# Optimization experiments

Hardware: AMD Instinct MI355X
Metric: run time of the kernel (lower is better)

The kernel has to match this reference:

```python
import jax, jax.numpy as jnp
import numpy as np

N_EMBED = 1024
HEAD_SIZE = 64


def setup_inputs() -> dict:
    key = jax.random.key(0)
    kx, kk, kq, kv = jax.random.split(key, 4)
    B, T = 8, 2048
    x = jax.random.normal(kx, (B, T, N_EMBED), dtype=jnp.float32)
    # nn.Linear weights, stored as (in, out) so projection is x @ W
    s = 1.0 / np.sqrt(N_EMBED)
    Wk = jax.random.uniform(kk, (N_EMBED, HEAD_SIZE), jnp.float32, -s, s)
    Wq = jax.random.uniform(kq, (N_EMBED, HEAD_SIZE), jnp.float32, -s, s)
    Wv = jax.random.uniform(kv, (N_EMBED, HEAD_SIZE), jnp.float32, -s, s)
    return {"x": x, "Wk": Wk, "Wq": Wq, "Wv": Wv}


def reference(x, Wk, Wq, Wv):
    # x: [B, T, C] with C = n_embed
    C = x.shape[-1]
    k = x @ Wk  # [B, T, H]
    q = x @ Wq  # [B, T, H]
    v = x @ Wv  # [B, T, H]
    # NOTE: original scales by n_embed**-0.5, not head_size**-0.5
    wei = jnp.einsum("bth,bsh->bts", q, k) * (C ** -0.5)  # [B, T, T]
    wei = jax.nn.softmax(wei, axis=-1)
    # dropout = 0.0 (eval mode) -> identity
    out = jnp.einsum("bts,bsh->bth", wei, v)  # [B, T, H]
    return out
```

## Files before the change

### kernel.cpp

```cpp
#include <hip/hip_runtime.h>
#include <stdint.h>


#define B_ 8
#define T_ 2048
#define C_ 1024
#define H_ 64

typedef float f32x4 __attribute__((ext_vector_type(4)));
typedef short s16x8 __attribute__((ext_vector_type(8)));

__device__ __forceinline__ unsigned int rhu16(float f) {
    return (__float_as_uint(f) + 0x8000u) >> 16;
}
__device__ __forceinline__ unsigned int pkbf(float lo, float hi) {
    unsigned int a = __float_as_uint(lo) + 0x8000u;
    unsigned int b = __float_as_uint(hi) + 0x8000u;
    return __builtin_amdgcn_perm(b, a, 0x07060302u);
}
__device__ __forceinline__ void ld_lds16(const void* g, void* l) {
    __builtin_amdgcn_global_load_lds(
        (const __attribute__((address_space(1))) unsigned int*)g,
        (__attribute__((address_space(3))) unsigned int*)l, 16, 0, 0);
}

__global__ __launch_bounds__(256) void wconv(const float* __restrict__ Wk,
        const float* __restrict__ Wq, const float* __restrict__ Wv,
        unsigned short* __restrict__ Wt) {
    __shared__ float ls[64 * 65];
    const int bx = blockIdx.x, t = threadIdx.x;
    const int mat = bx >> 4, c0 = (bx & 15) << 6;
    const float* W = (mat == 0) ? Wk : ((mat == 1) ? Wq : Wv);
    const float sc = (mat == 1) ? 0.03125f : 1.0f;
    #pragma unroll
    for (int k = 0; k < 4; k++) {
        int i = t + (k << 8);
        int cr = i >> 4, hq = (i & 15) << 2;
        float4 v = *reinterpret_cast<const float4*>(&W[(size_t)(c0 + cr) * H_ + hq]);
        ls[cr * 65 + hq + 0] = v.x; ls[cr * 65 + hq + 1] = v.y;
        ls[cr * 65 + hq + 2] = v.z; ls[cr * 65 + hq + 3] = v.w;
    }
    __syncthreads();
    #pragma unroll
    for (int k = 0; k < 4; k++) {
        int i = t + (k << 8);
        int h = i >> 4, cq = (i & 15) << 2;
        float a = ls[(cq + 0) * 65 + h] * sc, b = ls[(cq + 1) * 65 + h] * sc;
        float c = ls[(cq + 2) * 65 + h] * sc, d = ls[(cq + 3) * 65 + h] * sc;
        uint2 o; o.x = pkbf(a, b); o.y = pkbf(c, d);
        *reinterpret_cast<uint2*>(&Wt[(size_t)(mat * 64 + h) * C_ + c0 + cq]) = o;
    }
}

__global__ __launch_bounds__(128, 2) void qkv(const float* __restrict__ x,
        const unsigned short* __restrict__ Wt,
        unsigned short* __restrict__ kb, unsigned short* __restrict__ qb,
        unsigned short* __restrict__ vtb) {
    const int t = threadIdx.x, lane = t & 63, w = t >> 6;
    const int l15 = lane & 15, quad = lane >> 4;
    const int m0 = blockIdx.x * 32;
    const int bb = m0 >> 11;
    const int colw = w * 96;

    const char* xq0 = (const char*)(x + (size_t)(m0 + l15) * C_ + quad * 8);
    const char* xq1 = xq0 + (size_t)16 * C_ * 4;
    const char* wq[6];
    #pragma unroll
    for (int ct = 0; ct < 6; ct++)
        wq[ct] = (const char*)(Wt + (size_t)(colw + ct * 16 + l15) * C_ + quad * 8);

    f32x4 acc[2][6];
    #pragma unroll
    for (int rt = 0; rt < 2; rt++)
        #pragma unroll
        for (int ct = 0; ct < 6; ct++)
            #pragma unroll
            for (int j = 0; j < 4; j++) acc[rt][ct][j] = 0.0f;

    float4 xr[3][2][2][2];
    #pragma unroll
    for (int cc = 0; cc < 2; cc++) {
        #pragma unroll
        for (int ks = 0; ks < 2; ks++)
            #pragma unroll
            for (int h = 0; h < 2; h++) {
                xr[cc][0][ks][h] = *reinterpret_cast<const float4*>(
                    xq0 + cc * 256 + ks * 128 + h * 16);
                xr[cc][1][ks][h] = *reinterpret_cast<const float4*>(
                    xq1 + cc * 256 + ks * 128 + h * 16);
            }
    }

    #pragma unroll
    for (int c = 0; c < 16; c++) {
        __builtin_amdgcn_sched_barrier(0);
        if (c < 14) {
            const int sl = (c + 2) % 3, off = (c + 2) * 256;
            #pragma unroll
            for (int ks = 0; ks < 2; ks++)
                #pragma unroll
                for (int h = 0; h < 2; h++) {
                    xr[sl][0][ks][h] = *reinterpret_cast<const float4*>(
                        xq0 + off + ks * 128 + h * 16);
                    xr[sl][1][ks][h] = *reinterpret_cast<const float4*>(
                        xq1 + off + ks * 128 + h * 16);
                }
        }
        uint4 wr[6][2];
        #pragma unroll
        for (int ct = 0; ct < 6; ct++)
            #pragma unroll
            for (int ks = 0; ks < 2; ks++)
                wr[ct][ks] = *reinterpret_cast<const uint4*>(
                    wq[ct] + c * 128 + ks * 64);
        __builtin_amdgcn_sched_barrier(0);

        const int cs = c % 3;
        s16x8 af[2][2];
        #pragma unroll
        for (int rt = 0; rt < 2; rt++)
            #pragma unroll
            for (int ks = 0; ks < 2; ks++) {
                const float4 a = xr[cs][rt][ks][0], b = xr[cs][rt][ks][1];
                uint4 pk;
                pk.x = pkbf(a.x, a.y); pk.y = pkbf(a.z, a.w);
                pk.z = pkbf(b.x, b.y); pk.w = pkbf(b.z, b.w);
                af[rt][ks] = *reinterpret_cast<s16x8*>(&pk);
            }
        #pragma unroll
        for (int ks = 0; ks < 2; ks++)
            #pragma unroll
            for (int rt = 0; rt < 2; rt++)
                #pragma unroll
                for (int ct = 0; ct < 6; ct++)
                    acc[rt][ct] = __builtin_amdgcn_mfma_f32_16x16x32_bf16(
                        af[rt][ks],
                        *reinterpret_cast<s16x8*>(&wr[ct][ks]),
                        acc[rt][ct], 0, 0, 0);
    }

    #pragma unroll
    for (int ct = 0; ct < 6; ct++) {
        int cb = colw + ct * 16;
        int sel = cb >> 6;
        int h = (cb & 63) + l15;
        #pragma unroll
        for (int rt = 0; rt < 2; rt++) {
            int row0 = m0 + rt * 16 + quad * 4;
            if (sel < 2) {
                unsigned short* dst = sel ? qb : kb;
                #pragma unroll
                for (int r = 0; r < 4; r++)
                    dst[(size_t)(row0 + r) * H_ + h] = (unsigned short)rhu16(acc[rt][ct][r]);
            } else {
                int tt = row0 - bb * T_;
                uint2 pk;
                pk.x = pkbf(acc[rt][ct][0], acc[rt][ct][1]);
                pk.y = pkbf(acc[rt][ct][2], acc[rt][ct][3]);
                *reinterpret_cast<uint2*>(&vtb[((size_t)bb * H_ + h) * T_ + tt]) = pk;
            }
        }
    }
}

__global__ __launch_bounds__(256, 2) void attn(
        const unsigned short* __restrict__ qb,
        const unsigned short* __restrict__ kb,
        const unsigned short* __restrict__ vtb,
        float* __restrict__ out) {
    __shared__ __align__(16) char smem[75776];

    const int t = threadIdx.x, lane = t & 63, w = t >> 6;
    const int l15 = lane & 15, quad = lane >> 4;
    const int bb = blockIdx.x & 7;
    const int q0 = (blockIdx.x >> 3) << 5;
    const size_t kbase = (size_t)bb * T_ * H_;
    char* Kb = smem + w * 16384;
    char* Vb = Kb + 8192;
    unsigned short* Pw = (unsigned short*)(smem + 65536 + w * 2560);

    s16x8 qf[2][2];
    #pragma unroll
    for (int rt = 0; rt < 2; rt++)
        #pragma unroll
        for (int ks = 0; ks < 2; ks++)
            qf[rt][ks] = *reinterpret_cast<const s16x8*>(
                &qb[kbase + (size_t)(q0 + rt * 16 + l15) * H_ + ks * 32 + quad * 8]);

    const unsigned short* kp = kb + kbase;
    const unsigned short* vp = vtb + (size_t)bb * H_ * T_;
    size_t kg[4], vg[4]; int kl[4], vl[4];
    #pragma unroll
    for (int g = 0; g < 4; g++) {
        kg[g] = (size_t)(g * 8 + (lane & 7)) * H_ + (lane >> 3) * 8;
        kl[g] = g * 1024 + lane * 16;
        vg[g] = (size_t)(g * 16 + l15) * T_ + quad * 8;
        vl[g] = g * 1024 + lane * 16;
    }

    const int sw = w << 9;
    #pragma unroll
    for (int g = 0; g < 4; g++) ld_lds16(kp + (size_t)sw * H_ + kg[g], Kb + kl[g]);
    #pragma unroll
    for (int g = 0; g < 4; g++) ld_lds16(vp + sw + vg[g], Vb + vl[g]);

    f32x4 oacc[2][4];
    #pragma unroll
    for (int rt = 0; rt < 2; rt++)
        #pragma unroll
        for (int ht = 0; ht < 4; ht++)
            #pragma unroll
            for (int j = 0; j < 4; j++) oacc[rt][ht][j] = 0.0f;
    float l_run[2] = {0.0f, 0.0f};
    const f32x4 z4 = {0.0f, 0.0f, 0.0f, 0.0f};

    for (int it = 0; it < 16; it++) {
        const int cb = it & 1;
        if (it < 15) {
            const int sn = sw + (it + 1) * 32;
            char* Kn = Kb + (cb ^ 1) * 4096;
            char* Vn = Vb + (cb ^ 1) * 4096;
            #pragma unroll
            for (int g = 0; g < 4; g++) ld_lds16(kp + (size_t)sn * H_ + kg[g], Kn + kl[g]);
            #pragma unroll
            for (int g = 0; g < 4; g++) ld_lds16(vp + sn + vg[g], Vn + vl[g]);
            __builtin_amdgcn_sched_barrier(0);
            __builtin_amdgcn_s_waitcnt(0x0f78);
        } else {
            __builtin_amdgcn_s_waitcnt(0x0f70);
        }
        __builtin_amdgcn_sched_barrier(0);

        const unsigned short* Kc = (const unsigned short*)(Kb + cb * 4096);
        const unsigned short* Vc = (const unsigned short*)(Vb + cb * 4096);

        s16x8 kf[2][2], vf[4];
        #pragma unroll
        for (int st = 0; st < 2; st++)
            #pragma unroll
            for (int ks = 0; ks < 2; ks++) {
                int s = st * 16 + l15;
                kf[st][ks] = *reinterpret_cast<const s16x8*>(
                    Kc + (s >> 3) * 512 + ((4 * ks + quad) * 8 + (s & 7)) * 8);
            }
        #pragma unroll
        for (int ht = 0; ht < 4; ht++)
            vf[ht] = *reinterpret_cast<const s16x8*>(
                Vc + ht * 512 + (quad * 16 + l15) * 8);

        f32x4 sacc[2][2];
        #pragma unroll
        for (int rt = 0; rt < 2; rt++)
            #pragma unroll
            for (int st = 0; st < 2; st++) {
                f32x4 s0v = __builtin_amdgcn_mfma_f32_16x16x32_bf16(kf[st][0], qf[rt][0], z4, 0, 0, 0);
                sacc[rt][st] = __builtin_amdgcn_mfma_f32_16x16x32_bf16(kf[st][1], qf[rt][1], s0v, 0, 0, 0);
            }

        #pragma unroll
        for (int rt = 0; rt < 2; rt++) {
            float ls = 0.0f;
            #pragma unroll
            for (int st = 0; st < 2; st++) {
                float p0 = __expf(sacc[rt][st][0]);
                float p1 = __expf(sacc[rt][st][1]);
                float p2 = __expf(sacc[rt][st][2]);
                float p3 = __expf(sacc[rt][st][3]);
                ls += (p0 + p1) + (p2 + p3);
                uint2 pk; pk.x = pkbf(p0, p1); pk.y = pkbf(p2, p3);
                *reinterpret_cast<uint2*>(
                    &Pw[(rt * 16 + l15) * 40 + st * 16 + quad * 4]) = pk;
            }
            l_run[rt] += ls;
        }

        #pragma unroll
        for (int rt = 0; rt < 2; rt++) {
            s16x8 pf = *reinterpret_cast<const s16x8*>(&Pw[(rt * 16 + l15) * 40 + quad * 8]);
            #pragma unroll
            for (int ht = 0; ht < 4; ht++)
                oacc[rt][ht] = __builtin_amdgcn_mfma_f32_16x16x32_bf16(
                    pf, vf[ht], oacc[rt][ht], 0, 0, 0);
        }
    }

    #pragma unroll
    for (int rt = 0; rt < 2; rt++) {
        l_run[rt] += __shfl_xor(l_run[rt], 16);
        l_run[rt] += __shfl_xor(l_run[rt], 32);
    }

    __syncthreads();
    float* Osf = (float*)smem;
    float* Ls  = (float*)smem + 3 * 32 * 66;
    if (w > 0) {
        int wi = w - 1;
        #pragma unroll
        for (int rt = 0; rt < 2; rt++) {
            if (quad == 0) Ls[wi * 32 + rt * 16 + l15] = l_run[rt];
            #pragma unroll
            for (int ht = 0; ht < 4; ht++)
                #pragma unroll
                for (int r = 0; r < 4; r++)
                    Osf[wi * 2112 + (rt * 16 + quad * 4 + r) * 66 + ht * 16 + l15] = oacc[rt][ht][r];
        }
    }
    __syncthreads();
    if (w == 0) {
        #pragma unroll
        for (int rt = 0; rt < 2; rt++)
            #pragma unroll
            for (int r = 0; r < 4; r++) {
                int row = rt * 16 + quad * 4 + r;
                float lt = __shfl(l_run[rt], quad * 4 + r)
                         + Ls[0 * 32 + row] + Ls[1 * 32 + row] + Ls[2 * 32 + row];
                float inv = 1.0f / lt;
                #pragma unroll
                for (int ht = 0; ht < 4; ht++) {
                    float o = oacc[rt][ht][r]
                            + Osf[0 * 2112 + row * 66 + ht * 16 + l15]
                            + Osf[1 * 2112 + row * 66 + ht * 16 + l15]
                            + Osf[2 * 2112 + row * 66 + ht * 16 + l15];
                    out[kbase + (size_t)(q0 + row) * H_ + ht * 16 + l15] = o * inv;
                }
            }
    }
}

extern "C" void kernel_launch(void* const* d_in, const int* in_sizes, int n_in,
                              void* d_out, int out_size, void* d_ws, size_t ws_size,
                              hipStream_t stream) {
    const float* x  = (const float*)d_in[0];
    const float* Wk = (const float*)d_in[1];
    const float* Wq = (const float*)d_in[2];
    const float* Wv = (const float*)d_in[3];

    unsigned short* kb  = (unsigned short*)d_ws;
    unsigned short* qbf = kb  + (size_t)B_ * T_ * H_;
    unsigned short* vtb = qbf + (size_t)B_ * T_ * H_;
    unsigned short* Wt  = (unsigned short*)d_out;

    wconv<<<48,  256, 0, stream>>>(Wk, Wq, Wv, Wt);
    qkv  <<<512, 128, 0, stream>>>(x, Wt, kb, qbf, vtb);
    attn <<<512, 256, 0, stream>>>(qbf, kb, vtb, (float*)d_out);
}
```

Baseline: 160.5 us.

## Load attention K/V fragments directly into registers and split qkv across four waves

The attention kernel drops the async global-to-LDS staging of K and V tiles and instead loads MFMA fragments straight from global memory into a double-buffered register set, prefetching two iterations ahead. This shrinks shared memory use, which may allow more blocks per CU. The qkv projection kernel moves to 256 threads with each wave owning a 16-row by 96-column tile, and it double-buffers both x and weight fragments in registers. The cost is more register pressure and less coalesced global loads, which now depend on cache hits instead of shared staging.

```diff
diff --git a/kernel.cpp b/kernel.cpp
--- a/kernel.cpp
+++ b/kernel.cpp
@@ -17,11 +17,6 @@
     unsigned int a = __float_as_uint(lo) + 0x8000u;
     unsigned int b = __float_as_uint(hi) + 0x8000u;
     return __builtin_amdgcn_perm(b, a, 0x07060302u);
-}
-__device__ __forceinline__ void ld_lds16(const void* g, void* l) {
-    __builtin_amdgcn_global_load_lds(
-        (const __attribute__((address_space(1))) unsigned int*)g,
-        (__attribute__((address_space(3))) unsigned int*)l, 16, 0, 0);
 }
 
 __global__ __launch_bounds__(256) void wconv(const float* __restrict__ Wk,
@@ -52,91 +47,80 @@
     }
 }
 
-__global__ __launch_bounds__(128, 2) void qkv(const float* __restrict__ x,
+__global__ __launch_bounds__(256, 2) void qkv(const float* __restrict__ x,
         const unsigned short* __restrict__ Wt,
         unsigned short* __restrict__ kb, unsigned short* __restrict__ qb,
         unsigned short* __restrict__ vtb) {
     const int t = threadIdx.x, lane = t & 63, w = t >> 6;
+    const int rw = w >> 1, cw = w & 1;
     const int l15 = lane & 15, quad = lane >> 4;
     const int m0 = blockIdx.x * 32;
     const int bb = m0 >> 11;
-    const int colw = w * 96;
-
-    const char* xq0 = (const char*)(x + (size_t)(m0 + l15) * C_ + quad * 8);
-    const char* xq1 = xq0 + (size_t)16 * C_ * 4;
-    const char* wq[6];
+    const int colw = cw * 96;
+
+    const char* xp = (const char*)(x + (size_t)(m0 + rw * 16 + l15) * C_ + quad * 8);
+    const char* wp[6];
     #pragma unroll
     for (int ct = 0; ct < 6; ct++)
-        wq[ct] = (const char*)(Wt + (size_t)(colw + ct * 16 + l15) * C_ + quad * 8);
-
-    f32x4 acc[2][6];
-    #pragma unroll
-    for (int rt = 0; rt < 2; rt++)
+        wp[ct] = (const char*)(Wt + (size_t)(colw + ct * 16 + l15) * C_ + quad * 8);
+
+    f32x4 acc[6];
+    #pragma unroll
+    for (int ct = 0; ct < 6; ct++)
+        #pragma unroll
+        for (int j = 0; j < 4; j++) acc[ct][j] = 0.0f;
+
+    float4 xr[2][4];
+    uint4  wr[2][6][2];
+
+    #pragma unroll
+    for (int p = 0; p < 2; p++) {
+        xr[p][0] = *reinterpret_cast<const float4*>(xp + p * 256 + 0);
+        xr[p][1] = *reinterpret_cast<const float4*>(xp + p * 256 + 16);
+        xr[p][2] = *reinterpret_cast<const float4*>(xp + p * 256 + 128);
+        xr[p][3] = *reinterpret_cast<const float4*>(xp + p * 256 + 144);
         #pragma unroll
         for (int ct = 0; ct < 6; ct++)
             #pragma unroll
-            for (int j = 0; j < 4; j++) acc[rt][ct][j] = 0.0f;
-
-    float4 xr[3][2][2][2];
-    #pragma unroll
-    for (int cc = 0; cc < 2; cc++) {
+            for (int ks = 0; ks < 2; ks++)
+                wr[p][ct][ks] = *reinterpret_cast<const uint4*>(
+                    wp[ct] + p * 128 + ks * 64);
+    }
+
+    #pragma unroll
+    for (int c = 0; c < 16; c++) {
+        const int cb = c & 1;
+        s16x8 af[2];
+        #pragma unroll
+        for (int ks = 0; ks < 2; ks++) {
+            const float4 a = xr[cb][ks * 2 + 0], b = xr[cb][ks * 2 + 1];
+            uint4 pk;
+            pk.x = pkbf(a.x, a.y); pk.y = pkbf(a.z, a.w);
+            pk.z = pkbf(b.x, b.y); pk.w = pkbf(b.z, b.w);
+            af[ks] = *reinterpret_cast<s16x8*>(&pk);
+        }
         #pragma unroll
         for (int ks = 0; ks < 2; ks++)
             #pragma unroll
-            for (int h = 0; h < 2; h++) {
-                xr[cc][0][ks][h] = *reinterpret_cast<const float4*>(
-                    xq0 + cc * 256 + ks * 128 + h * 16);
-                xr[cc][1][ks][h] = *reinterpret_cast<const float4*>(
-                    xq1 + cc * 256 + ks * 128 + h * 16);
-            }
-    }
-
-    #pragma unroll
-    for (int c = 0; c < 16; c++) {
+            for (int ct = 0; ct < 6; ct++)
+                acc[ct] = __builtin_amdgcn_mfma_f32_16x16x32_bf16(
+                    af[ks], *reinterpret_cast<s16x8*>(&wr[cb][ct][ks]),
+                    acc[ct], 0, 0, 0);
         __builtin_amdgcn_sched_barrier(0);
         if (c < 14) {
-            const int sl = (c + 2) % 3, off = (c + 2) * 256;
-            #pragma unroll
-            for (int ks = 0; ks < 2; ks++)
+            const int o = (c + 2) * 256, ow = (c + 2) * 128;
+            xr[cb][0] = *reinterpret_cast<const float4*>(xp + o + 0);
+            xr[cb][1] = *reinterpret_cast<const float4*>(xp + o + 16);
+            xr[cb][2] = *reinterpret_cast<const float4*>(xp + o + 128);
+            xr[cb][3] = *reinterpret_cast<const float4*>(xp + o + 144);
+            #pragma unroll
+            for (int ct = 0; ct < 6; ct++)
                 #pragma unroll
-                for (int h = 0; h < 2; h++) {
-                    xr[sl][0][ks][h] = *reinterpret_cast<const float4*>(
-                        xq0 + off + ks * 128 + h * 16);
-                    xr[sl][1][ks][h] = *reinterpret_cast<const float4*>(
-                        xq1 + off + ks * 128 + h * 16);
-                }
-        }
-        uint4 wr[6][2];
-        #pragma unroll
-        for (int ct = 0; ct < 6; ct++)
-            #pragma unroll
-            for (int ks = 0; ks < 2; ks++)
-                wr[ct][ks] = *reinterpret_cast<const uint4*>(
-                    wq[ct] + c * 128 + ks * 64);
+                for (int ks = 0; ks < 2; ks++)
+                    wr[cb][ct][ks] = *reinterpret_cast<const uint4*>(
+                        wp[ct] + ow + ks * 64);
+        }
         __builtin_amdgcn_sched_barrier(0);
-
-        const int cs = c % 3;
-        s16x8 af[2][2];
-        #pragma unroll
-        for (int rt = 0; rt < 2; rt++)
-            #pragma unroll
-            for (int ks = 0; ks < 2; ks++) {
-                const float4 a = xr[cs][rt][ks][0], b = xr[cs][rt][ks][1];
-                uint4 pk;
-                pk.x = pkbf(a.x, a.y); pk.y = pkbf(a.z, a.w);
-                pk.z = pkbf(b.x, b.y); pk.w = pkbf(b.z, b.w);
-                af[rt][ks] = *reinterpret_cast<s16x8*>(&pk);
-            }
-        #pragma unroll
-        for (int ks = 0; ks < 2; ks++)
-            #pragma unroll
-            for (int rt = 0; rt < 2; rt++)
-                #pragma unroll
-                for (int ct = 0; ct < 6; ct++)
-                    acc[rt][ct] = __builtin_amdgcn_mfma_f32_16x16x32_bf16(
-                        af[rt][ks],
-                        *reinterpret_cast<s16x8*>(&wr[ct][ks]),
-                        acc[rt][ct], 0, 0, 0);
     }
 
     #pragma unroll
@@ -144,21 +128,18 @@
         int cb = colw + ct * 16;
         int sel = cb >> 6;
         int h = (cb & 63) + l15;
-        #pragma unroll
-        for (int rt = 0; rt < 2; rt++) {
-            int row0 = m0 + rt * 16 + quad * 4;
-            if (sel < 2) {
-                unsigned short* dst = sel ? qb : kb;
-                #pragma unroll
-                for (int r = 0; r < 4; r++)
-                    dst[(size_t)(row0 + r) * H_ + h] = (unsigned short)rhu16(acc[rt][ct][r]);
-            } else {
-                int tt = row0 - bb * T_;
-                uint2 pk;
-                pk.x = pkbf(acc[rt][ct][0], acc[rt][ct][1]);
-                pk.y = pkbf(acc[rt][ct][2], acc[rt][ct][3]);
-                *reinterpret_cast<uint2*>(&vtb[((size_t)bb * H_ + h) * T_ + tt]) = pk;
-            }
+        int row0 = m0 + rw * 16 + quad * 4;
+        if (sel < 2) {
+            unsigned short* dst = sel ? qb : kb;
+            #pragma unroll
+            for (int r = 0; r < 4; r++)
+                dst[(size_t)(row0 + r) * H_ + h] = (unsigned short)rhu16(acc[ct][r]);
+        } else {
+            int tt = row0 - bb * T_;
+            uint2 pk;
+            pk.x = pkbf(acc[ct][0], acc[ct][1]);
+            pk.y = pkbf(acc[ct][2], acc[ct][3]);
+            *reinterpret_cast<uint2*>(&vtb[((size_t)bb * H_ + h) * T_ + tt]) = pk;
         }
     }
 }
@@ -168,16 +149,14 @@
         const unsigned short* __restrict__ kb,
         const unsigned short* __restrict__ vtb,
         float* __restrict__ out) {
-    __shared__ __align__(16) char smem[75776];
+    __shared__ __align__(16) char smem[25728];
 
     const int t = threadIdx.x, lane = t & 63, w = t >> 6;
     const int l15 = lane & 15, quad = lane >> 4;
     const int bb = blockIdx.x & 7;
     const int q0 = (blockIdx.x >> 3) << 5;
     const size_t kbase = (size_t)bb * T_ * H_;
-    char* Kb = smem + w * 16384;
-    char* Vb = Kb + 8192;
-    unsigned short* Pw = (unsigned short*)(smem + 65536 + w * 2560);
+    unsigned short* Pw = (unsigned short*)(smem + w * 2560);
 
     s16x8 qf[2][2];
     #pragma unroll
@@ -187,22 +166,27 @@
             qf[rt][ks] = *reinterpret_cast<const s16x8*>(
                 &qb[kbase + (size_t)(q0 + rt * 16 + l15) * H_ + ks * 32 + quad * 8]);
 
-    const unsigned short* kp = kb + kbase;
-    const unsigned short* vp = vtb + (size_t)bb * H_ * T_;
-    size_t kg[4], vg[4]; int kl[4], vl[4];
-    #pragma unroll
-    for (int g = 0; g < 4; g++) {
-        kg[g] = (size_t)(g * 8 + (lane & 7)) * H_ + (lane >> 3) * 8;
-        kl[g] = g * 1024 + lane * 16;
-        vg[g] = (size_t)(g * 16 + l15) * T_ + quad * 8;
-        vl[g] = g * 1024 + lane * 16;
-    }
-
     const int sw = w << 9;
-    #pragma unroll
-    for (int g = 0; g < 4; g++) ld_lds16(kp + (size_t)sw * H_ + kg[g], Kb + kl[g]);
-    #pragma unroll
-    for (int g = 0; g < 4; g++) ld_lds16(vp + sw + vg[g], Vb + vl[g]);
+    const unsigned short* kq = kb + kbase + (size_t)(sw + l15) * H_ + quad * 8;
+    const unsigned short* vq[4];
+    #pragma unroll
+    for (int ht = 0; ht < 4; ht++)
+        vq[ht] = vtb + ((size_t)bb * H_ + ht * 16 + l15) * T_ + sw + quad * 8;
+
+    s16x8 kfb[2][2][2], vfb[2][4];
+    #pragma unroll
+    for (int p = 0; p < 2; p++) {
+        const unsigned short* kc = kq + (size_t)p * 2048;
+        #pragma unroll
+        for (int st = 0; st < 2; st++)
+            #pragma unroll
+            for (int ks = 0; ks < 2; ks++)
+                kfb[p][st][ks] = *reinterpret_cast<const s16x8*>(
+                    kc + st * 1024 + ks * 32);
+        #pragma unroll
+        for (int ht = 0; ht < 4; ht++)
+            vfb[p][ht] = *reinterpret_cast<const s16x8*>(vq[ht] + p * 32);
+    }
 
     f32x4 oacc[2][4];
     #pragma unroll
@@ -214,47 +198,19 @@
     float l_run[2] = {0.0f, 0.0f};
     const f32x4 z4 = {0.0f, 0.0f, 0.0f, 0.0f};
 
+    #pragma unroll
     for (int it = 0; it < 16; it++) {
         const int cb = it & 1;
-        if (it < 15) {
-            const int sn = sw + (it + 1) * 32;
-            char* Kn = Kb + (cb ^ 1) * 4096;
-            char* Vn = Vb + (cb ^ 1) * 4096;
-            #pragma unroll
-            for (int g = 0; g < 4; g++) ld_lds16(kp + (size_t)sn * H_ + kg[g], Kn + kl[g]);
-            #pragma unroll
-            for (int g = 0; g < 4; g++) ld_lds16(vp + sn + vg[g], Vn + vl[g]);
-            __builtin_amdgcn_sched_barrier(0);
-            __builtin_amdgcn_s_waitcnt(0x0f78);
-        } else {
-            __builtin_amdgcn_s_waitcnt(0x0f70);
-        }
-        __builtin_amdgcn_sched_barrier(0);
-
-        const unsigned short* Kc = (const unsigned short*)(Kb + cb * 4096);
-        const unsigned short* Vc = (const unsigned short*)(Vb + cb * 4096);
-
-        s16x8 kf[2][2], vf[4];
-        #pragma unroll
-        for (int st = 0; st < 2; st++)
-            #pragma unroll
-            for (int ks = 0; ks < 2; ks++) {
-                int s = st * 16 + l15;
-                kf[st][ks] = *reinterpret_cast<const s16x8*>(
-                    Kc + (s >> 3) * 512 + ((4 * ks + quad) * 8 + (s & 7)) * 8);
-            }
-        #pragma unroll
-        for (int ht = 0; ht < 4; ht++)
-            vf[ht] = *reinterpret_cast<const s16x8*>(
-                Vc + ht * 512 + (quad * 16 + l15) * 8);
 
         f32x4 sacc[2][2];
         #pragma unroll
         for (int rt = 0; rt < 2; rt++)
             #pragma unroll
             for (int st = 0; st < 2; st++) {
-                f32x4 s0v = __builtin_amdgcn_mfma_f32_16x16x32_bf16(kf[st][0], qf[rt][0], z4, 0, 0, 0);
-                sacc[rt][st] = __builtin_amdgcn_mfma_f32_16x16x32_bf16(kf[st][1], qf[rt][1], s0v, 0, 0, 0);
+                f32x4 s0v = __builtin_amdgcn_mfma_f32_16x16x32_bf16(
+                    kfb[cb][st][0], qf[rt][0], z4, 0, 0, 0);
+                sacc[rt][st] = __builtin_amdgcn_mfma_f32_16x16x32_bf16(
+                    kfb[cb][st][1], qf[rt][1], s0v, 0, 0, 0);
             }
 
         #pragma unroll
@@ -276,12 +232,29 @@
 
         #pragma unroll
         for (int rt = 0; rt < 2; rt++) {
-            s16x8 pf = *reinterpret_cast<const s16x8*>(&Pw[(rt * 16 + l15) * 40 + quad * 8]);
+            s16x8 pf = *reinterpret_cast<const s16x8*>(
+                &Pw[(rt * 16 + l15) * 40 + quad * 8]);
             #pragma unroll
             for (int ht = 0; ht < 4; ht++)
                 oacc[rt][ht] = __builtin_amdgcn_mfma_f32_16x16x32_bf16(
-                    pf, vf[ht], oacc[rt][ht], 0, 0, 0);
-        }
+                    pf, vfb[cb][ht], oacc[rt][ht], 0, 0, 0);
+        }
+
+        __builtin_amdgcn_sched_barrier(0);
+        if (it < 14) {
+            const unsigned short* kc = kq + (size_t)(it + 2) * 2048;
+            #pragma unroll
+            for (int st = 0; st < 2; st++)
+                #pragma unroll
+                for (int ks = 0; ks < 2; ks++)
+                    kfb[cb][st][ks] = *reinterpret_cast<const s16x8*>(
+                        kc + st * 1024 + ks * 32);
+            #pragma unroll
+            for (int ht = 0; ht < 4; ht++)
+                vfb[cb][ht] = *reinterpret_cast<const s16x8*>(
+                    vq[ht] + (it + 2) * 32);
+        }
+        __builtin_amdgcn_sched_barrier(0);
     }
 
     #pragma unroll
@@ -341,6 +314,6 @@
     unsigned short* Wt  = (unsigned short*)d_out;
 
     wconv<<<48,  256, 0, stream>>>(Wk, Wq, Wv, Wt);
-    qkv  <<<512, 128, 0, stream>>>(x, Wt, kb, qbf, vtb);
+    qkv  <<<512, 256, 0, stream>>>(x, Wt, kb, qbf, vtb);
     attn <<<512, 256, 0, stream>>>(qbf, kb, vtb, (float*)d_out);
 }
```

Result: slower. 179.0 us (+11.5%).
